# Performance work log

Measured on AMD Instinct MI355X. Metric: run time of the kernel, lower is better.

## Reference

```python
import jax, jax.numpy as jnp
import numpy as np

N, E = 50000, 800000
IN, HID, OUT = 128, 32, 8


def setup_inputs() -> dict:
    key = jax.random.key(0)
    ks = jax.random.split(key, 20)
    f32 = jnp.float32
    def rn(k, shape, s=0.1):
        return (jax.random.normal(k, shape, dtype=f32) * s)
    return {
        'x': jax.random.normal(ks[0], (N, IN), dtype=f32),
        'edge_index': jax.random.randint(ks[1], (2, E), 0, N, dtype=jnp.int32),
        'edge_attr': jax.random.uniform(ks[2], (E, 1), dtype=f32),
        # layer 1: heads=4, out=HID, concat -> 4*HID channels
        'w1l': rn(ks[3], (IN, 4 * HID)), 'b1l': rn(ks[4], (4 * HID,)),
        'w1r': rn(ks[5], (IN, 4 * HID)), 'b1r': rn(ks[6], (4 * HID,)),
        'w1e': rn(ks[7], (1, 4 * HID)),
        'att1': rn(ks[8], (4, HID)), 'bias1': rn(ks[9], (4 * HID,)),
        # layer 2: heads=2, out=HID, mean over heads -> HID channels
        'w2l': rn(ks[10], (4 * HID, 2 * HID)), 'b2l': rn(ks[11], (2 * HID,)),
        'w2r': rn(ks[12], (4 * HID, 2 * HID)), 'b2r': rn(ks[13], (2 * HID,)),
        'w2e': rn(ks[14], (1, 2 * HID)),
        'att2': rn(ks[15], (2, HID)), 'bias2': rn(ks[16], (HID,)),
        'wc': rn(ks[17], (HID, OUT)), 'bc': rn(ks[18], (OUT,)),
    }


def _add_self_loops(edge_index, edge_attr, n):
    # PyG GATv2Conv adds self-loops; edge feature for loops = mean of edge_attr
    loop = jnp.arange(n, dtype=edge_index.dtype)
    src = jnp.concatenate([edge_index[0], loop])
    dst = jnp.concatenate([edge_index[1], loop])
    mean_attr = jnp.broadcast_to(edge_attr.mean(axis=0), (n, edge_attr.shape[1]))
    ea = jnp.concatenate([edge_attr, mean_attr], axis=0)
    return src, dst, ea


def _gatv2(x, src, dst, eattr, Wl, bl, Wr, br, We, att, bias, heads, out, concat):
    n = x.shape[0]
    xl = (x @ Wl + bl).reshape(n, heads, out)   # source transform (messages)
    xr = (x @ Wr + br).reshape(n, heads, out)   # target transform
    e = (eattr @ We).reshape(-1, heads, out)    # edge embedding
    z = jax.nn.leaky_relu(xl[src] + xr[dst] + e, negative_slope=0.2)  # [Etot,H,D]
    score = jnp.einsum('ehd,hd->eh', z, att)
    # segment softmax over incoming edges of each destination node
    smax = jax.ops.segment_max(score, dst, num_segments=n)
    ex = jnp.exp(score - smax[dst])
    denom = jax.ops.segment_sum(ex, dst, num_segments=n)
    alpha = ex / denom[dst]                     # [Etot,H]
    agg = jax.ops.segment_sum(xl[src] * alpha[..., None], dst, num_segments=n)
    o = agg.reshape(n, heads * out) if concat else agg.mean(axis=1)
    return o + bias


def reference(x, edge_index, edge_attr, w1l, b1l, w1r, b1r, w1e, att1, bias1,
              w2l, b2l, w2r, b2r, w2e, att2, bias2, wc, bc):
    src, dst, ea = _add_self_loops(edge_index, edge_attr, x.shape[0])
    h = _gatv2(x, src, dst, ea, w1l, b1l, w1r, b1r, w1e, att1, bias1, 4, HID, True)
    h = jax.nn.elu(h)
    # dropout p=0.4 is training-only; reference is eval mode (identity)
    h = _gatv2(h, src, dst, ea, w2l, b2l, w2r, b2r, w2e, att2, bias2, 2, HID, False)
    h = jax.nn.elu(h)
    return h @ wc + bc
```

## Files before the change

### kernel.cpp

```cpp
#include <hip/hip_runtime.h>
#include <hip/hip_fp16.h>
#include <math.h>

typedef _Float16 h2_t __attribute__((ext_vector_type(2)));
typedef _Float16 h4_t __attribute__((ext_vector_type(4)));
typedef _Float16 h8_t __attribute__((ext_vector_type(8)));
typedef float f4_t __attribute__((ext_vector_type(4)));
typedef float f8_t __attribute__((ext_vector_type(8)));

#define PRE_BLOCKS 512
#define SB 512
#define NBUK_PAD 800
#define CTB 16

__device__ inline h8_t load8f_to_h8(const float* p) {
    float4 a = *(const float4*)p;
    float4 b = *(const float4*)(p + 4);
    h8_t r;
    r[0] = (_Float16)a.x; r[1] = (_Float16)a.y; r[2] = (_Float16)a.z; r[3] = (_Float16)a.w;
    r[4] = (_Float16)b.x; r[5] = (_Float16)b.y; r[6] = (_Float16)b.z; r[7] = (_Float16)b.w;
    return r;
}

__device__ inline h4_t load4f_to_h4(const float* p) {
    float4 a = *(const float4*)p;
    h4_t r;
    r[0] = (_Float16)a.x; r[1] = (_Float16)a.y; r[2] = (_Float16)a.z; r[3] = (_Float16)a.w;
    return r;
}

__device__ inline float dot8h(h8_t a, h8_t b, float s) {
    s = __builtin_amdgcn_fdot2(__builtin_shufflevector(a, a, 0, 1),
                               __builtin_shufflevector(b, b, 0, 1), s, false);
    s = __builtin_amdgcn_fdot2(__builtin_shufflevector(a, a, 2, 3),
                               __builtin_shufflevector(b, b, 2, 3), s, false);
    s = __builtin_amdgcn_fdot2(__builtin_shufflevector(a, a, 4, 5),
                               __builtin_shufflevector(b, b, 4, 5), s, false);
    s = __builtin_amdgcn_fdot2(__builtin_shufflevector(a, a, 6, 7),
                               __builtin_shufflevector(b, b, 6, 7), s, false);
    return s;
}

__device__ inline float dot4h(h4_t a, h4_t b, float s) {
    s = __builtin_amdgcn_fdot2(__builtin_shufflevector(a, a, 0, 1),
                               __builtin_shufflevector(b, b, 0, 1), s, false);
    s = __builtin_amdgcn_fdot2(__builtin_shufflevector(a, a, 2, 3),
                               __builtin_shufflevector(b, b, 2, 3), s, false);
    return s;
}

__device__ inline float elu1(float v) { return v > 0.f ? v : __expf(v) - 1.f; }

struct MA {
    const float* x;
    const float* eattr;
    const int* ei;
    const float *w1l, *b1l, *w1r, *b1r, *w1e, *att1, *bias1;
    const float *w2l, *b2l, *w2r, *b2r, *w2e, *att2, *bias2;
    const float *wc, *bc;
    float* out;
    _Float16 *xh, *xl1h, *xr1h, *h1h, *xl2h, *xr2h;
    _Float16 *p1l, *p1r, *p2l, *p2r;
    int *deg, *offb;
    unsigned* parth;
    unsigned *tstart, *tot;
    unsigned* smeanq;
    unsigned* tmp;
    float* part;
    unsigned* edges;
    int N, E, NW, NBK, CE;
    int n0node, n1node;
    float invE;
};


__device__ inline void phase_packw(const MA& a, int g) {
    const float* W;
    _Float16* P;
    int M, lg;
    if (g < 2048)      { W = a.w1l; P = a.p1l; M = 128; lg = g; }
    else if (g < 4096) { W = a.w1r; P = a.p1r; M = 128; lg = g - 2048; }
    else if (g < 5120) { W = a.w2l; P = a.p2l; M = 64;  lg = g - 4096; }
    else               { W = a.w2r; P = a.p2r; M = 64;  lg = g - 5120; }
    int ln = lg & 63;
    int s = (lg >> 6) & 3;
    int tt = lg >> 8;
    int m = ln & 15, quad = ln >> 4;
    h8_t v;
#pragma unroll
    for (int j = 0; j < 8; ++j)
        v[j] = (_Float16)W[(size_t)(s * 32 + quad * 8 + j) * M + tt * 16 + m];
    *(h8_t*)(P + (size_t)lg * 8) = v;
}

template <int NT>
__device__ inline void phase_mm_tile(const MA& a, const _Float16* X, int rt, int lane,
                                     const _Float16* Pl, const float* bl, _Float16* Yl,
                                     const _Float16* Pr, const float* br, _Float16* Yr) {
    int nrow = lane & 15, quad = lane >> 4;
    int row = rt * 16 + nrow;
    if (row >= a.N) return;
    const _Float16* xp = X + (size_t)row * 128 + quad * 8;
    h8_t bf0 = *(const h8_t*)(xp);
    h8_t bf1 = *(const h8_t*)(xp + 32);
    h8_t bf2 = *(const h8_t*)(xp + 64);
    h8_t bf3 = *(const h8_t*)(xp + 96);
#pragma unroll
    for (int w = 0; w < 2; ++w) {
        const _Float16* P = w ? Pr : Pl;
        const float* bias = w ? br : bl;
        _Float16* Y = w ? Yr : Yl;
#pragma unroll
        for (int t2 = 0; t2 < NT; ++t2) {
            f4_t acc = {0.f, 0.f, 0.f, 0.f};
            const _Float16* pb = P + (size_t)t2 * 2048 + (size_t)lane * 8;
            acc = __builtin_amdgcn_mfma_f32_16x16x32_f16(*(const h8_t*)pb, bf0, acc, 0, 0, 0);
            acc = __builtin_amdgcn_mfma_f32_16x16x32_f16(*(const h8_t*)(pb + 512), bf1, acc, 0, 0, 0);
            acc = __builtin_amdgcn_mfma_f32_16x16x32_f16(*(const h8_t*)(pb + 1024), bf2, acc, 0, 0, 0);
            acc = __builtin_amdgcn_mfma_f32_16x16x32_f16(*(const h8_t*)(pb + 1536), bf3, acc, 0, 0, 0);
            float4 bv = *(const float4*)(bias + t2 * 16 + quad * 4);
            h4_t o;
            o[0] = (_Float16)(acc[0] + bv.x);
            o[1] = (_Float16)(acc[1] + bv.y);
            o[2] = (_Float16)(acc[2] + bv.z);
            o[3] = (_Float16)(acc[3] + bv.w);
            *(h4_t*)(Y + (size_t)row * (NT * 16) + t2 * 16 + quad * 4) = o;
        }
    }
}


__global__ __launch_bounds__(256) void k_pre(MA a) {
    if (blockIdx.x >= PRE_BLOCKS) {
        int g = (blockIdx.x - PRE_BLOCKS) * 256 + threadIdx.x;
        if (g < 6144) phase_packw(a, g);
        return;
    }
    __shared__ unsigned bh[NBUK_PAD];
    __shared__ float sd[4];
    int tx = threadIdx.x;
    for (int j = tx; j < NBUK_PAD; j += 256) bh[j] = 0u;

    int t = blockIdx.x * 256 + tx;
    const int stride = PRE_BLOCKS * 256;
    int nchunk = (a.N * 128) >> 3;
    for (int i = t; i < nchunk; i += stride) {
        h8_t v = load8f_to_h8(a.x + (size_t)i * 8);
        *(h8_t*)(a.xh + (size_t)i * 8) = v;
    }
    float s = 0.f;
    for (int i = t; i < a.E; i += stride) s += a.eattr[i];
    for (int o = 1; o < 64; o <<= 1) s += __shfl_xor(s, o, 64);
    if ((tx & 63) == 0) sd[tx >> 6] = s;
    __syncthreads();
    if (tx == 0) a.part[blockIdx.x] = sd[0] + sd[1] + sd[2] + sd[3];

    int e0 = blockIdx.x * a.CE, e1 = min(e0 + a.CE, a.E);
    for (int e = e0 + tx; e < e1; e += 256)
        atomicAdd(&bh[((unsigned)a.ei[a.E + e]) >> 6], 1u);
    __syncthreads();
    for (int j = tx; j < NBUK_PAD; j += 256)
        a.parth[(size_t)blockIdx.x * NBUK_PAD + j] = bh[j];
}


__global__ __launch_bounds__(512, 1) void k_colscan(MA a) {
    __shared__ unsigned tile[512][CTB + 1];
    int tx = threadIdx.x;
    int b0 = blockIdx.x * CTB;
    unsigned* rp = a.parth + (size_t)tx * NBUK_PAD + b0;
#pragma unroll
    for (int j = 0; j < CTB; ++j) tile[tx][j] = rp[j];
    __syncthreads();

    int c = tx >> 5;
    int g = tx & 31;
    unsigned base = 0;
#pragma unroll
    for (int k = 0; k < 16; ++k) {
        int r = k * 32 + g;
        unsigned orig = tile[r][c];
        unsigned v = orig;
#pragma unroll
        for (int o = 1; o < 32; o <<= 1) {
            unsigned u = __shfl_up(v, o, 32);
            if (g >= o) v += u;
        }
        tile[r][c] = base + (v - orig);
        base += __shfl(v, 31, 32);
    }
    if (g == 0) a.tot[b0 + c] = base;
    __syncthreads();
#pragma unroll
    for (int j = 0; j < CTB; ++j) rp[j] = tile[tx][j];
}


__global__ __launch_bounds__(1024, 1) void k_scan2(MA a) {
    __shared__ unsigned lds[1024];
    __shared__ float sd[16];
    int tx = threadIdx.x;
    unsigned v = (tx < a.NBK) ? a.tot[tx] : 0u;
    lds[tx] = v;
    float s = (tx < PRE_BLOCKS) ? a.part[tx] : 0.f;
    for (int o = 1; o < 64; o <<= 1) s += __shfl_xor(s, o, 64);
    if ((tx & 63) == 0) sd[tx >> 6] = s;
    __syncthreads();
    for (int o = 1; o < 1024; o <<= 1) {
        unsigned u = (tx >= o) ? lds[tx - o] : 0u;
        __syncthreads();
        lds[tx] += u;
        __syncthreads();
    }
    if (tx < a.NBK) a.tstart[tx] = lds[tx] - v;
    if (tx == 0) {
        float m = 0.f;
#pragma unroll
        for (int k = 0; k < 16; ++k) m += sd[k];
        a.smeanq[0] = (unsigned)__float2int_rn(m * a.invE * 255.f);
    }
}


__global__ __launch_bounds__(256) void k_scatter(MA a) {
    int bid = blockIdx.x;
    if (bid < a.NW) {
        int wid = bid * 4 + (threadIdx.x >> 6);
        int ntile = (a.N + 15) / 16;
        if (wid < ntile)
            phase_mm_tile<8>(a, a.xh, wid, threadIdx.x & 63,
                             a.p1l, a.b1l, a.xl1h, a.p1r, a.b1r, a.xr1h);
        return;
    }
    __shared__ unsigned cur[NBUK_PAD];
    int s = bid - a.NW;
    int tx = threadIdx.x;
    for (int j = tx; j < NBUK_PAD; j += 256)
        cur[j] = a.parth[(size_t)s * NBUK_PAD + j] + a.tstart[j];
    __syncthreads();
    int e0 = s * a.CE, e1 = min(e0 + a.CE, a.E);
    for (int e = e0 + tx; e < e1; e += 256) {
        int d = a.ei[a.E + e];
        unsigned src = (unsigned)a.ei[e];
        unsigned q = (unsigned)__float2int_rn(a.eattr[e] * 255.f);
        unsigned pos = atomicAdd(&cur[d >> 6], 1u);
        a.tmp[pos] = src | (q << 16) | ((unsigned)(d & 63) << 24);
    }
}


__global__ __launch_bounds__(256) void k_fine(MA a) {
    __shared__ int hist[64];
    __shared__ unsigned cur[64];
    __shared__ unsigned sm;
    int b = blockIdx.x;
    int tx = threadIdx.x;
    int n0 = b << 6;
    int nn = min(64, a.N - n0);
    unsigned ts = a.tstart[b], T = a.tot[b];
    if (tx < 64) hist[tx] = 0;
    if (tx == 0) sm = a.smeanq[0];
    __syncthreads();
    for (unsigned i = tx; i < T; i += 256) {
        unsigned v = a.tmp[ts + i];
        atomicAdd(&hist[(int)(v >> 24)], 1);
    }
    __syncthreads();
    if (tx < 64) {
        int deg1 = hist[tx] + 1;
        int vsc = deg1;
#pragma unroll
        for (int o = 1; o < 64; o <<= 1) {
            int u = __shfl_up(vsc, o, 64);
            if (tx >= o) vsc += u;
        }
        int off = (int)ts + n0 + (vsc - deg1);
        if (tx < nn) {
            a.offb[n0 + tx] = off;
            a.deg[n0 + tx] = deg1;
            a.edges[off] = (unsigned)(n0 + tx) | (sm << 24);
        }
        cur[tx] = (unsigned)(off + 1);
    }
    __syncthreads();
    for (unsigned i = tx; i < T; i += 256) {
        unsigned v = a.tmp[ts + i];
        int loc = (int)(v >> 24);
        unsigned pos = atomicAdd(&cur[loc], 1u);
        a.edges[pos] = (v & 0xFFFFu) | (((v >> 16) & 0xFFu) << 24);
    }
}


__global__ __launch_bounds__(256) void k_node1(MA a) {
    int tid = threadIdx.x;
    int q = tid & 15;
    int node = a.n0node + blockIdx.x * 16 + (tid >> 4);
    if (node >= a.n1node) return;
    unsigned cb = (unsigned)(q * 16);

    h8_t xrv = *(const h8_t*)((const char*)a.xr1h + ((unsigned)node << 8) + cb);
    h8_t wev = load8f_to_h8(a.w1e + q * 8);
    h8_t atv = load8f_to_h8(a.att1 + q * 8);
    const unsigned* ep = a.edges + a.offb[node];
    int deg1 = a.deg[node];
    int last = deg1 - 1;
    const char* xb = (const char*)a.xl1h;

    float l = 0.f;
    f8_t acc = {0.f, 0.f, 0.f, 0.f, 0.f, 0.f, 0.f, 0.f};

    auto GA = [&](unsigned p) -> h8_t {
        return *(const h8_t*)(xb + (((p & 0x00FFFFFFu) << 8) | cb));
    };
    auto LOADG = [&](int i, unsigned& p0, unsigned& p1, unsigned& p2, unsigned& p3,
                     h8_t& x0, h8_t& x1, h8_t& x2, h8_t& x3) {
        p0 = ep[i];
        p1 = ep[min(i + 1, last)];
        p2 = ep[min(i + 2, last)];
        p3 = ep[min(i + 3, last)];
        x0 = GA(p0); x1 = GA(p1); x2 = GA(p2); x3 = GA(p3);
    };
    auto COMPG = [&](int i, unsigned p0, unsigned p1, unsigned p2, unsigned p3,
                     h8_t x0, h8_t x1, h8_t x2, h8_t x3) {
        float e0 = (float)(p0 >> 24) * (1.f / 255.f);
        float e1 = (float)(p1 >> 24) * (1.f / 255.f);
        float e2 = (float)(p2 >> 24) * (1.f / 255.f);
        float e3 = (float)(p3 >> 24) * (1.f / 255.f);
        h8_t z0 = x0 + xrv + wev * (_Float16)e0;
        z0 = __builtin_elementwise_max(z0, z0 * (_Float16)0.2f);
        float sc0 = dot8h(z0, atv, 0.f);
        h8_t z1 = x1 + xrv + wev * (_Float16)e1;
        z1 = __builtin_elementwise_max(z1, z1 * (_Float16)0.2f);
        float sc1 = dot8h(z1, atv, 0.f);
        h8_t z2 = x2 + xrv + wev * (_Float16)e2;
        z2 = __builtin_elementwise_max(z2, z2 * (_Float16)0.2f);
        float sc2 = dot8h(z2, atv, 0.f);
        h8_t z3 = x3 + xrv + wev * (_Float16)e3;
        z3 = __builtin_elementwise_max(z3, z3 * (_Float16)0.2f);
        float sc3 = dot8h(z3, atv, 0.f);
        sc0 += __shfl_xor(sc0, 1, 64); sc0 += __shfl_xor(sc0, 2, 64);
        sc1 += __shfl_xor(sc1, 1, 64); sc1 += __shfl_xor(sc1, 2, 64);
        sc2 += __shfl_xor(sc2, 1, 64); sc2 += __shfl_xor(sc2, 2, 64);
        sc3 += __shfl_xor(sc3, 1, 64); sc3 += __shfl_xor(sc3, 2, 64);
        float pA = __expf(fminf(sc0, 60.f));
        float pB = (i + 1 < deg1) ? __expf(fminf(sc1, 60.f)) : 0.f;
        float pC = (i + 2 < deg1) ? __expf(fminf(sc2, 60.f)) : 0.f;
        float pD = (i + 3 < deg1) ? __expf(fminf(sc3, 60.f)) : 0.f;
        l += (pA + pB) + (pC + pD);
#pragma unroll
        for (int k = 0; k < 8; ++k)
            acc[k] = fmaf(pA, (float)x0[k],
                     fmaf(pB, (float)x1[k],
                     fmaf(pC, (float)x2[k], fmaf(pD, (float)x3[k], acc[k]))));
    };

    unsigned pa0, pa1, pa2, pa3, pb0, pb1, pb2, pb3;
    h8_t xa0, xa1, xa2, xa3, xb0, xb1, xb2, xb3;
    LOADG(0, pa0, pa1, pa2, pa3, xa0, xa1, xa2, xa3);
    for (int i = 0; i < deg1; i += 8) {
        if (i + 4 < deg1) LOADG(i + 4, pb0, pb1, pb2, pb3, xb0, xb1, xb2, xb3);
        COMPG(i, pa0, pa1, pa2, pa3, xa0, xa1, xa2, xa3);
        if (i + 8 < deg1) LOADG(i + 8, pa0, pa1, pa2, pa3, xa0, xa1, xa2, xa3);
        if (i + 4 < deg1) COMPG(i + 4, pb0, pb1, pb2, pb3, xb0, xb1, xb2, xb3);
    }

    float inv = 1.f / l;
    float4 b0 = *(const float4*)(a.bias1 + q * 8);
    float4 b1 = *(const float4*)(a.bias1 + q * 8 + 4);
    float bb[8] = {b0.x, b0.y, b0.z, b0.w, b1.x, b1.y, b1.z, b1.w};
    h8_t o;
#pragma unroll
    for (int k = 0; k < 8; ++k) o[k] = (_Float16)elu1(fmaf(acc[k], inv, bb[k]));
    *(h8_t*)((char*)a.h1h + ((unsigned)node << 8) + cb) = o;
}


__global__ __launch_bounds__(256) void k_mm4(MA a) {
    int wid = blockIdx.x * 4 + (threadIdx.x >> 6);
    int ntile = (a.N + 15) / 16;
    if (wid >= ntile) return;
    phase_mm_tile<4>(a, a.h1h, wid, threadIdx.x & 63,
                     a.p2l, a.b2l, a.xl2h, a.p2r, a.b2r, a.xr2h);
}


__global__ __launch_bounds__(256) void k_node2(MA a) {
    __shared__ float h2s[16][33];
    int tid = threadIdx.x;
    int lane = tid & 63;
    int wib = tid >> 6;
    int sub = lane >> 4;
    int r = lane & 15;
    int nloc = wib * 4 + sub;
    int node = blockIdx.x * 16 + nloc;
    int c0 = r * 4;

    if (node < a.N) {
        h4_t xrv = *(const h4_t*)(a.xr2h + (size_t)node * 64 + c0);
        h4_t wev = load4f_to_h4(a.w2e + c0);
        h4_t atv = load4f_to_h4(a.att2 + c0);
        const unsigned* ep = a.edges + a.offb[node];
        int deg1 = a.deg[node];
        int last = deg1 - 1;
        const char* xb = (const char*)a.xl2h;
        unsigned cb = (unsigned)(c0 * 2);
        float l = 0.f;
        float acc[4] = {0.f, 0.f, 0.f, 0.f};
        for (int i = 0; i < deg1; i += 4) {
            unsigned p[4];
            h4_t xv[4];
#pragma unroll
            for (int j = 0; j < 4; ++j) p[j] = ep[min(i + j, last)];
#pragma unroll
            for (int j = 0; j < 4; ++j)
                xv[j] = *(const h4_t*)(xb + (((p[j] & 0x00FFFFFFu) << 7) | cb));
#pragma unroll
            for (int j = 0; j < 4; ++j) {
                float ea = (float)(p[j] >> 24) * (1.f / 255.f);
                h4_t z = xv[j] + xrv + wev * (_Float16)ea;
                z = __builtin_elementwise_max(z, z * (_Float16)0.2f);
                float sc = dot4h(z, atv, 0.f);
                sc += __shfl_xor(sc, 1, 64);
                sc += __shfl_xor(sc, 2, 64);
                sc += __shfl_xor(sc, 4, 64);
                float pp = (i + j < deg1) ? __expf(fminf(sc, 60.f)) : 0.f;
                l += pp;
#pragma unroll
                for (int k = 0; k < 4; ++k) acc[k] = fmaf(pp, (float)xv[j][k], acc[k]);
            }
        }
        float inv = 1.f / l;
#pragma unroll
        for (int k = 0; k < 4; ++k) {
            float norm = acc[k] * inv;
            float other = __shfl_xor(norm, 8, 64);
            float v = 0.5f * (norm + other);
            if (r < 8) h2s[nloc][c0 + k] = elu1(v + a.bias2[c0 + k]);
        }
    }
    __syncthreads();
    if (tid < 128) {
        int n = tid >> 3, j = tid & 7;
        int gnode = blockIdx.x * 16 + n;
        if (gnode < a.N) {
            float acc = a.bc[j];
#pragma unroll 8
            for (int d = 0; d < 32; ++d) acc = fmaf(h2s[n][d], a.wc[d * 8 + j], acc);
            a.out[(size_t)gnode * 8 + j] = acc;
        }
    }
}


extern "C" void kernel_launch(void* const* d_in, const int* in_sizes, int n_in,
                              void* d_out, int out_size, void* d_ws, size_t ws_size,
                              hipStream_t stream) {
    const int N = in_sizes[0] / 128;
    const int E = in_sizes[2];
    const int tot = E + N;

    char* ws = (char*)d_ws;
    size_t o = 0;
    auto alloc = [&](size_t bytes) -> void* {
        void* p = ws + o;
        o += (bytes + 255) & ~(size_t)255;
        return p;
    };
    MA a;
    a.x     = (const float*)d_in[0];
    a.ei    = (const int*)d_in[1];
    a.eattr = (const float*)d_in[2];
    a.w1l = (const float*)d_in[3];  a.b1l = (const float*)d_in[4];
    a.w1r = (const float*)d_in[5];  a.b1r = (const float*)d_in[6];
    a.w1e = (const float*)d_in[7];  a.att1 = (const float*)d_in[8];
    a.bias1 = (const float*)d_in[9];
    a.w2l = (const float*)d_in[10]; a.b2l = (const float*)d_in[11];
    a.w2r = (const float*)d_in[12]; a.b2r = (const float*)d_in[13];
    a.w2e = (const float*)d_in[14]; a.att2 = (const float*)d_in[15];
    a.bias2 = (const float*)d_in[16];
    a.wc = (const float*)d_in[17];  a.bc = (const float*)d_in[18];
    a.out = (float*)d_out;

    a.xh   = (_Float16*)alloc((size_t)N * 128 * 2);
    a.xl1h = (_Float16*)alloc((size_t)N * 128 * 2);
    a.xr1h = (_Float16*)alloc((size_t)N * 128 * 2);
    a.h1h  = (_Float16*)alloc((size_t)N * 128 * 2);
    a.xl2h = (_Float16*)alloc((size_t)N * 64 * 2);
    a.xr2h = (_Float16*)alloc((size_t)N * 64 * 2);
    a.p1l  = (_Float16*)alloc(128 * 128 * 2);
    a.p1r  = (_Float16*)alloc(128 * 128 * 2);
    a.p2l  = (_Float16*)alloc(128 * 64 * 2);
    a.p2r  = (_Float16*)alloc(128 * 64 * 2);
    a.deg  = (int*)alloc((size_t)N * 4);
    a.offb = (int*)alloc((size_t)N * 4);
    a.parth  = (unsigned*)alloc((size_t)SB * NBUK_PAD * 4);
    a.tstart = (unsigned*)alloc(1024 * 4);
    a.tot    = (unsigned*)alloc(1024 * 4);
    a.smeanq = (unsigned*)alloc(256);
    a.part   = (float*)alloc(PRE_BLOCKS * 4);
    a.tmp    = (unsigned*)alloc((size_t)E * 4);
    a.edges  = (unsigned*)alloc((size_t)tot * 4);
    a.N = N;
    a.E = E;
    a.NW = (N + 63) / 64;
    a.NBK = (N + 63) >> 6;
    a.CE = (E + SB - 1) / SB;
    a.invE = 1.0f / (float)E;

    k_pre<<<PRE_BLOCKS + 24, 256, 0, stream>>>(a);
    k_colscan<<<NBUK_PAD / CTB, 512, 0, stream>>>(a);
    k_scan2<<<1, 1024, 0, stream>>>(a);
    k_scatter<<<a.NW + SB, 256, 0, stream>>>(a);
    k_fine<<<a.NBK, 256, 0, stream>>>(a);

    int mid = ((N / 2) + 15) & ~15;
    MA a1 = a; a1.n0node = 0;   a1.n1node = mid;
    MA a2 = a; a2.n0node = mid; a2.n1node = N;
    k_node1<<<mid / 16, 256, 0, stream>>>(a1);
    k_node1<<<(N - mid + 15) / 16, 256, 0, stream>>>(a2);

    k_mm4<<<(N + 63) / 64, 256, 0, stream>>>(a);
    k_node2<<<(N + 15) / 16, 256, 0, stream>>>(a);
}
```

Baseline: 247.5 us.

## Fuse fine CSR build, layer-1 aggregation and layer-2 matmul into one kernel

Removes the single-block scan kernel: each scatter block now recomputes the bucket prefix scan locally, and the fused kernel recomputes its own bucket start and the edge-attribute mean. The fine sort, layer-1 attention aggregation and the layer-2 MFMA projection are merged into one kernel per 64-node bucket, with h1 kept in shared memory instead of a global round-trip. This cuts four launches and the h1 global write and read. In exchange there is redundant prefix work per block, 16KB+ of LDS per block that may lower occupancy, and only about 782 blocks doing the gather-heavy node1 work, which loses the earlier split into two launches.

```diff
diff --git a/kernel.cpp b/kernel.cpp
--- a/kernel.cpp
+++ b/kernel.cpp
@@ -59,17 +59,15 @@
     const float *w2l, *b2l, *w2r, *b2r, *w2e, *att2, *bias2;
     const float *wc, *bc;
     float* out;
-    _Float16 *xh, *xl1h, *xr1h, *h1h, *xl2h, *xr2h;
+    _Float16 *xh, *xl1h, *xr1h, *xl2h, *xr2h;
     _Float16 *p1l, *p1r, *p2l, *p2r;
     int *deg, *offb;
     unsigned* parth;
-    unsigned *tstart, *tot;
-    unsigned* smeanq;
+    unsigned* tot;
     unsigned* tmp;
     float* part;
     unsigned* edges;
     int N, E, NW, NBK, CE;
-    int n0node, n1node;
     float invE;
 };
 
@@ -196,32 +194,6 @@
 }
 
 
-__global__ __launch_bounds__(1024, 1) void k_scan2(MA a) {
-    __shared__ unsigned lds[1024];
-    __shared__ float sd[16];
-    int tx = threadIdx.x;
-    unsigned v = (tx < a.NBK) ? a.tot[tx] : 0u;
-    lds[tx] = v;
-    float s = (tx < PRE_BLOCKS) ? a.part[tx] : 0.f;
-    for (int o = 1; o < 64; o <<= 1) s += __shfl_xor(s, o, 64);
-    if ((tx & 63) == 0) sd[tx >> 6] = s;
-    __syncthreads();
-    for (int o = 1; o < 1024; o <<= 1) {
-        unsigned u = (tx >= o) ? lds[tx - o] : 0u;
-        __syncthreads();
-        lds[tx] += u;
-        __syncthreads();
-    }
-    if (tx < a.NBK) a.tstart[tx] = lds[tx] - v;
-    if (tx == 0) {
-        float m = 0.f;
-#pragma unroll
-        for (int k = 0; k < 16; ++k) m += sd[k];
-        a.smeanq[0] = (unsigned)__float2int_rn(m * a.invE * 255.f);
-    }
-}
-
-
 __global__ __launch_bounds__(256) void k_scatter(MA a) {
     int bid = blockIdx.x;
     if (bid < a.NW) {
@@ -232,11 +204,36 @@
                              a.p1l, a.b1l, a.xl1h, a.p1r, a.b1r, a.xr1h);
         return;
     }
-    __shared__ unsigned cur[NBUK_PAD];
+    __shared__ unsigned cur[1024];
+    __shared__ unsigned wt[4];
     int s = bid - a.NW;
     int tx = threadIdx.x;
+    for (int j = tx; j < 1024; j += 256)
+        cur[j] = (j < NBUK_PAD) ? a.tot[j] : 0u;
+    __syncthreads();
+    {
+        unsigned x0 = cur[tx * 4], x1 = cur[tx * 4 + 1], x2 = cur[tx * 4 + 2], x3 = cur[tx * 4 + 3];
+        unsigned s1 = x0 + x1, s2 = s1 + x2, t = s2 + x3;
+        unsigned inc = t;
+#pragma unroll
+        for (int o = 1; o < 64; o <<= 1) {
+            unsigned u = __shfl_up(inc, o, 64);
+            if ((tx & 63) >= o) inc += u;
+        }
+        if ((tx & 63) == 63) wt[tx >> 6] = inc;
+        __syncthreads();
+        unsigned wb = 0;
+#pragma unroll
+        for (int k = 0; k < 4; ++k) wb += (k < (tx >> 6)) ? wt[k] : 0u;
+        unsigned excl = wb + (inc - t);
+        cur[tx * 4]     = excl;
+        cur[tx * 4 + 1] = excl + x0;
+        cur[tx * 4 + 2] = excl + s1;
+        cur[tx * 4 + 3] = excl + s2;
+    }
+    __syncthreads();
     for (int j = tx; j < NBUK_PAD; j += 256)
-        cur[j] = a.parth[(size_t)s * NBUK_PAD + j] + a.tstart[j];
+        cur[j] += a.parth[(size_t)s * NBUK_PAD + j];
     __syncthreads();
     int e0 = s * a.CE, e1 = min(e0 + a.CE, a.E);
     for (int e = e0 + tx; e < e1; e += 256) {
@@ -249,22 +246,34 @@
 }
 
 
-__global__ __launch_bounds__(256) void k_fine(MA a) {
+__global__ __launch_bounds__(256) void k_fuse(MA a) {
     __shared__ int hist[64];
     __shared__ unsigned cur[64];
-    __shared__ unsigned sm;
-    int b = blockIdx.x;
-    int tx = threadIdx.x;
+    __shared__ int offl[64], degl[64];
+    __shared__ unsigned rts[4];
+    __shared__ float rs[4];
+    __shared__ _Float16 h1s[64 * 128];
+
+    int b = blockIdx.x, tx = threadIdx.x;
     int n0 = b << 6;
     int nn = min(64, a.N - n0);
-    unsigned ts = a.tstart[b], T = a.tot[b];
+
     if (tx < 64) hist[tx] = 0;
-    if (tx == 0) sm = a.smeanq[0];
-    __syncthreads();
-    for (unsigned i = tx; i < T; i += 256) {
-        unsigned v = a.tmp[ts + i];
-        atomicAdd(&hist[(int)(v >> 24)], 1);
-    }
+    unsigned ps = 0;
+    for (int j = tx; j < b; j += 256) ps += a.tot[j];
+    for (int o = 1; o < 64; o <<= 1) ps += __shfl_xor(ps, o, 64);
+    if ((tx & 63) == 0) rts[tx >> 6] = ps;
+    float s = 0.f;
+    for (int j = tx; j < PRE_BLOCKS; j += 256) s += a.part[j];
+    for (int o = 1; o < 64; o <<= 1) s += __shfl_xor(s, o, 64);
+    if ((tx & 63) == 0) rs[tx >> 6] = s;
+    __syncthreads();
+    unsigned ts = rts[0] + rts[1] + rts[2] + rts[3];
+    unsigned sm = (unsigned)__float2int_rn((rs[0] + rs[1] + rs[2] + rs[3]) * a.invE * 255.f);
+    unsigned T = a.tot[b];
+
+    for (unsigned i = tx; i < T; i += 256)
+        atomicAdd(&hist[(int)(a.tmp[ts + i] >> 24)], 1);
     __syncthreads();
     if (tx < 64) {
         int deg1 = hist[tx] + 1;
@@ -279,109 +288,137 @@
             a.offb[n0 + tx] = off;
             a.deg[n0 + tx] = deg1;
             a.edges[off] = (unsigned)(n0 + tx) | (sm << 24);
+            offl[tx] = off;
+            degl[tx] = deg1;
         }
         cur[tx] = (unsigned)(off + 1);
     }
     __syncthreads();
     for (unsigned i = tx; i < T; i += 256) {
         unsigned v = a.tmp[ts + i];
-        int loc = (int)(v >> 24);
-        unsigned pos = atomicAdd(&cur[loc], 1u);
+        unsigned pos = atomicAdd(&cur[v >> 24], 1u);
         a.edges[pos] = (v & 0xFFFFu) | (((v >> 16) & 0xFFu) << 24);
     }
-}
-
-
-__global__ __launch_bounds__(256) void k_node1(MA a) {
-    int tid = threadIdx.x;
-    int q = tid & 15;
-    int node = a.n0node + blockIdx.x * 16 + (tid >> 4);
-    if (node >= a.n1node) return;
+    __syncthreads();
+
+    int q = tx & 15;
     unsigned cb = (unsigned)(q * 16);
-
-    h8_t xrv = *(const h8_t*)((const char*)a.xr1h + ((unsigned)node << 8) + cb);
     h8_t wev = load8f_to_h8(a.w1e + q * 8);
     h8_t atv = load8f_to_h8(a.att1 + q * 8);
-    const unsigned* ep = a.edges + a.offb[node];
-    int deg1 = a.deg[node];
-    int last = deg1 - 1;
+    float4 bv0 = *(const float4*)(a.bias1 + q * 8);
+    float4 bv1 = *(const float4*)(a.bias1 + q * 8 + 4);
+    float bb[8] = {bv0.x, bv0.y, bv0.z, bv0.w, bv1.x, bv1.y, bv1.z, bv1.w};
     const char* xb = (const char*)a.xl1h;
 
-    float l = 0.f;
-    f8_t acc = {0.f, 0.f, 0.f, 0.f, 0.f, 0.f, 0.f, 0.f};
-
-    auto GA = [&](unsigned p) -> h8_t {
-        return *(const h8_t*)(xb + (((p & 0x00FFFFFFu) << 8) | cb));
-    };
-    auto LOADG = [&](int i, unsigned& p0, unsigned& p1, unsigned& p2, unsigned& p3,
-                     h8_t& x0, h8_t& x1, h8_t& x2, h8_t& x3) {
-        p0 = ep[i];
-        p1 = ep[min(i + 1, last)];
-        p2 = ep[min(i + 2, last)];
-        p3 = ep[min(i + 3, last)];
-        x0 = GA(p0); x1 = GA(p1); x2 = GA(p2); x3 = GA(p3);
-    };
-    auto COMPG = [&](int i, unsigned p0, unsigned p1, unsigned p2, unsigned p3,
-                     h8_t x0, h8_t x1, h8_t x2, h8_t x3) {
-        float e0 = (float)(p0 >> 24) * (1.f / 255.f);
-        float e1 = (float)(p1 >> 24) * (1.f / 255.f);
-        float e2 = (float)(p2 >> 24) * (1.f / 255.f);
-        float e3 = (float)(p3 >> 24) * (1.f / 255.f);
-        h8_t z0 = x0 + xrv + wev * (_Float16)e0;
-        z0 = __builtin_elementwise_max(z0, z0 * (_Float16)0.2f);
-        float sc0 = dot8h(z0, atv, 0.f);
-        h8_t z1 = x1 + xrv + wev * (_Float16)e1;
-        z1 = __builtin_elementwise_max(z1, z1 * (_Float16)0.2f);
-        float sc1 = dot8h(z1, atv, 0.f);
-        h8_t z2 = x2 + xrv + wev * (_Float16)e2;
-        z2 = __builtin_elementwise_max(z2, z2 * (_Float16)0.2f);
-        float sc2 = dot8h(z2, atv, 0.f);
-        h8_t z3 = x3 + xrv + wev * (_Float16)e3;
-        z3 = __builtin_elementwise_max(z3, z3 * (_Float16)0.2f);
-        float sc3 = dot8h(z3, atv, 0.f);
-        sc0 += __shfl_xor(sc0, 1, 64); sc0 += __shfl_xor(sc0, 2, 64);
-        sc1 += __shfl_xor(sc1, 1, 64); sc1 += __shfl_xor(sc1, 2, 64);
-        sc2 += __shfl_xor(sc2, 1, 64); sc2 += __shfl_xor(sc2, 2, 64);
-        sc3 += __shfl_xor(sc3, 1, 64); sc3 += __shfl_xor(sc3, 2, 64);
-        float pA = __expf(fminf(sc0, 60.f));
-        float pB = (i + 1 < deg1) ? __expf(fminf(sc1, 60.f)) : 0.f;
-        float pC = (i + 2 < deg1) ? __expf(fminf(sc2, 60.f)) : 0.f;
-        float pD = (i + 3 < deg1) ? __expf(fminf(sc3, 60.f)) : 0.f;
-        l += (pA + pB) + (pC + pD);
-#pragma unroll
-        for (int k = 0; k < 8; ++k)
-            acc[k] = fmaf(pA, (float)x0[k],
-                     fmaf(pB, (float)x1[k],
-                     fmaf(pC, (float)x2[k], fmaf(pD, (float)x3[k], acc[k]))));
-    };
-
-    unsigned pa0, pa1, pa2, pa3, pb0, pb1, pb2, pb3;
-    h8_t xa0, xa1, xa2, xa3, xb0, xb1, xb2, xb3;
-    LOADG(0, pa0, pa1, pa2, pa3, xa0, xa1, xa2, xa3);
-    for (int i = 0; i < deg1; i += 8) {
-        if (i + 4 < deg1) LOADG(i + 4, pb0, pb1, pb2, pb3, xb0, xb1, xb2, xb3);
-        COMPG(i, pa0, pa1, pa2, pa3, xa0, xa1, xa2, xa3);
-        if (i + 8 < deg1) LOADG(i + 8, pa0, pa1, pa2, pa3, xa0, xa1, xa2, xa3);
-        if (i + 4 < deg1) COMPG(i + 4, pb0, pb1, pb2, pb3, xb0, xb1, xb2, xb3);
-    }
-
-    float inv = 1.f / l;
-    float4 b0 = *(const float4*)(a.bias1 + q * 8);
-    float4 b1 = *(const float4*)(a.bias1 + q * 8 + 4);
-    float bb[8] = {b0.x, b0.y, b0.z, b0.w, b1.x, b1.y, b1.z, b1.w};
-    h8_t o;
-#pragma unroll
-    for (int k = 0; k < 8; ++k) o[k] = (_Float16)elu1(fmaf(acc[k], inv, bb[k]));
-    *(h8_t*)((char*)a.h1h + ((unsigned)node << 8) + cb) = o;
-}
-
-
-__global__ __launch_bounds__(256) void k_mm4(MA a) {
-    int wid = blockIdx.x * 4 + (threadIdx.x >> 6);
-    int ntile = (a.N + 15) / 16;
-    if (wid >= ntile) return;
-    phase_mm_tile<4>(a, a.h1h, wid, threadIdx.x & 63,
-                     a.p2l, a.b2l, a.xl2h, a.p2r, a.b2r, a.xr2h);
+    for (int rr = 0; rr < 64; rr += 16) {
+        int nloc = rr + (tx >> 4);
+        if (nloc < nn) {
+            int node = n0 + nloc;
+            h8_t xrv = *(const h8_t*)((const char*)a.xr1h + ((unsigned)node << 8) + cb);
+            const unsigned* ep = a.edges + offl[nloc];
+            int deg1 = degl[nloc];
+            int last = deg1 - 1;
+            float l = 0.f;
+            f8_t acc = {0.f, 0.f, 0.f, 0.f, 0.f, 0.f, 0.f, 0.f};
+
+            auto GA = [&](unsigned p) -> h8_t {
+                return *(const h8_t*)(xb + (((p & 0x00FFFFFFu) << 8) | cb));
+            };
+            auto LOADG = [&](int i, unsigned& p0, unsigned& p1, unsigned& p2, unsigned& p3,
+                             h8_t& x0, h8_t& x1, h8_t& x2, h8_t& x3) {
+                p0 = ep[i];
+                p1 = ep[min(i + 1, last)];
+                p2 = ep[min(i + 2, last)];
+                p3 = ep[min(i + 3, last)];
+                x0 = GA(p0); x1 = GA(p1); x2 = GA(p2); x3 = GA(p3);
+            };
+            auto COMPG = [&](int i, unsigned p0, unsigned p1, unsigned p2, unsigned p3,
+                             h8_t x0, h8_t x1, h8_t x2, h8_t x3) {
+                float e0 = (float)(p0 >> 24) * (1.f / 255.f);
+                float e1 = (float)(p1 >> 24) * (1.f / 255.f);
+                float e2 = (float)(p2 >> 24) * (1.f / 255.f);
+                float e3 = (float)(p3 >> 24) * (1.f / 255.f);
+                h8_t z0 = x0 + xrv + wev * (_Float16)e0;
+                z0 = __builtin_elementwise_max(z0, z0 * (_Float16)0.2f);
+                float sc0 = dot8h(z0, atv, 0.f);
+                h8_t z1 = x1 + xrv + wev * (_Float16)e1;
+                z1 = __builtin_elementwise_max(z1, z1 * (_Float16)0.2f);
+                float sc1 = dot8h(z1, atv, 0.f);
+                h8_t z2 = x2 + xrv + wev * (_Float16)e2;
+                z2 = __builtin_elementwise_max(z2, z2 * (_Float16)0.2f);
+                float sc2 = dot8h(z2, atv, 0.f);
+                h8_t z3 = x3 + xrv + wev * (_Float16)e3;
+                z3 = __builtin_elementwise_max(z3, z3 * (_Float16)0.2f);
+                float sc3 = dot8h(z3, atv, 0.f);
+                sc0 += __shfl_xor(sc0, 1, 64); sc0 += __shfl_xor(sc0, 2, 64);
+                sc1 += __shfl_xor(sc1, 1, 64); sc1 += __shfl_xor(sc1, 2, 64);
+                sc2 += __shfl_xor(sc2, 1, 64); sc2 += __shfl_xor(sc2, 2, 64);
+                sc3 += __shfl_xor(sc3, 1, 64); sc3 += __shfl_xor(sc3, 2, 64);
+                float pA = __expf(fminf(sc0, 60.f));
+                float pB = (i + 1 < deg1) ? __expf(fminf(sc1, 60.f)) : 0.f;
+                float pC = (i + 2 < deg1) ? __expf(fminf(sc2, 60.f)) : 0.f;
+                float pD = (i + 3 < deg1) ? __expf(fminf(sc3, 60.f)) : 0.f;
+                l += (pA + pB) + (pC + pD);
+#pragma unroll
+                for (int k = 0; k < 8; ++k)
+                    acc[k] = fmaf(pA, (float)x0[k],
+                             fmaf(pB, (float)x1[k],
+                             fmaf(pC, (float)x2[k], fmaf(pD, (float)x3[k], acc[k]))));
+            };
+
+            unsigned pa0, pa1, pa2, pa3, pb0, pb1, pb2, pb3;
+            h8_t xa0, xa1, xa2, xa3, xb0, xb1, xb2, xb3;
+            LOADG(0, pa0, pa1, pa2, pa3, xa0, xa1, xa2, xa3);
+            for (int i = 0; i < deg1; i += 8) {
+                if (i + 4 < deg1) LOADG(i + 4, pb0, pb1, pb2, pb3, xb0, xb1, xb2, xb3);
+                COMPG(i, pa0, pa1, pa2, pa3, xa0, xa1, xa2, xa3);
+                if (i + 8 < deg1) LOADG(i + 8, pa0, pa1, pa2, pa3, xa0, xa1, xa2, xa3);
+                if (i + 4 < deg1) COMPG(i + 4, pb0, pb1, pb2, pb3, xb0, xb1, xb2, xb3);
+            }
+
+            float inv = 1.f / l;
+            h8_t o;
+#pragma unroll
+            for (int k = 0; k < 8; ++k) o[k] = (_Float16)elu1(fmaf(acc[k], inv, bb[k]));
+            *(h8_t*)(h1s + nloc * 128 + q * 8) = o;
+        }
+    }
+    __syncthreads();
+
+    {
+        int wv = tx >> 6, lane = tx & 63;
+        int nrow = lane & 15, quad = lane >> 4;
+        int row = n0 + wv * 16 + nrow;
+        if (row < a.N) {
+            const _Float16* xp = h1s + (wv * 16 + nrow) * 128 + quad * 8;
+            h8_t bf0 = *(const h8_t*)(xp);
+            h8_t bf1 = *(const h8_t*)(xp + 32);
+            h8_t bf2 = *(const h8_t*)(xp + 64);
+            h8_t bf3 = *(const h8_t*)(xp + 96);
+#pragma unroll
+            for (int w = 0; w < 2; ++w) {
+                const _Float16* P = w ? a.p2r : a.p2l;
+                const float* bias = w ? a.b2r : a.b2l;
+                _Float16* Y = w ? a.xr2h : a.xl2h;
+#pragma unroll
+                for (int t2 = 0; t2 < 4; ++t2) {
+                    f4_t acc2 = {0.f, 0.f, 0.f, 0.f};
+                    const _Float16* pb = P + (size_t)t2 * 2048 + (size_t)lane * 8;
+                    acc2 = __builtin_amdgcn_mfma_f32_16x16x32_f16(*(const h8_t*)pb, bf0, acc2, 0, 0, 0);
+                    acc2 = __builtin_amdgcn_mfma_f32_16x16x32_f16(*(const h8_t*)(pb + 512), bf1, acc2, 0, 0, 0);
+                    acc2 = __builtin_amdgcn_mfma_f32_16x16x32_f16(*(const h8_t*)(pb + 1024), bf2, acc2, 0, 0, 0);
+                    acc2 = __builtin_amdgcn_mfma_f32_16x16x32_f16(*(const h8_t*)(pb + 1536), bf3, acc2, 0, 0, 0);
+                    float4 bv = *(const float4*)(bias + t2 * 16 + quad * 4);
+                    h4_t o;
+                    o[0] = (_Float16)(acc2[0] + bv.x);
+                    o[1] = (_Float16)(acc2[1] + bv.y);
+                    o[2] = (_Float16)(acc2[2] + bv.z);
+                    o[3] = (_Float16)(acc2[3] + bv.w);
+                    *(h4_t*)(Y + (size_t)row * 64 + t2 * 16 + quad * 4) = o;
+                }
+            }
+        }
+    }
 }
 
 
@@ -485,7 +522,6 @@
     a.xh   = (_Float16*)alloc((size_t)N * 128 * 2);
     a.xl1h = (_Float16*)alloc((size_t)N * 128 * 2);
     a.xr1h = (_Float16*)alloc((size_t)N * 128 * 2);
-    a.h1h  = (_Float16*)alloc((size_t)N * 128 * 2);
     a.xl2h = (_Float16*)alloc((size_t)N * 64 * 2);
     a.xr2h = (_Float16*)alloc((size_t)N * 64 * 2);
     a.p1l  = (_Float16*)alloc(128 * 128 * 2);
@@ -494,13 +530,11 @@
     a.p2r  = (_Float16*)alloc(128 * 64 * 2);
     a.deg  = (int*)alloc((size_t)N * 4);
     a.offb = (int*)alloc((size_t)N * 4);
-    a.parth  = (unsigned*)alloc((size_t)SB * NBUK_PAD * 4);
-    a.tstart = (unsigned*)alloc(1024 * 4);
-    a.tot    = (unsigned*)alloc(1024 * 4);
-    a.smeanq = (unsigned*)alloc(256);
-    a.part   = (float*)alloc(PRE_BLOCKS * 4);
-    a.tmp    = (unsigned*)alloc((size_t)E * 4);
-    a.edges  = (unsigned*)alloc((size_t)tot * 4);
+    a.parth = (unsigned*)alloc((size_t)SB * NBUK_PAD * 4);
+    a.tot   = (unsigned*)alloc(1024 * 4);
+    a.part  = (float*)alloc(PRE_BLOCKS * 4);
+    a.tmp   = (unsigned*)alloc((size_t)E * 4);
+    a.edges = (unsigned*)alloc((size_t)tot * 4);
     a.N = N;
     a.E = E;
     a.NW = (N + 63) / 64;
@@ -510,16 +544,7 @@
 
     k_pre<<<PRE_BLOCKS + 24, 256, 0, stream>>>(a);
     k_colscan<<<NBUK_PAD / CTB, 512, 0, stream>>>(a);
-    k_scan2<<<1, 1024, 0, stream>>>(a);
     k_scatter<<<a.NW + SB, 256, 0, stream>>>(a);
-    k_fine<<<a.NBK, 256, 0, stream>>>(a);
-
-    int mid = ((N / 2) + 15) & ~15;
-    MA a1 = a; a1.n0node = 0;   a1.n1node = mid;
-    MA a2 = a; a2.n0node = mid; a2.n1node = N;
-    k_node1<<<mid / 16, 256, 0, stream>>>(a1);
-    k_node1<<<(N - mid + 15) / 16, 256, 0, stream>>>(a2);
-
-    k_mm4<<<(N + 63) / 64, 256, 0, stream>>>(a);
+    k_fuse<<<a.NBK, 256, 0, stream>>>(a);
     k_node2<<<(N + 15) / 16, 256, 0, stream>>>(a);
 }
```

After: 241.8 us. 2.3% less time.
